# Kernel optimization log

Measured on AMD Instinct MI355X. Metric: run time of the kernel, lower is better.

## Reference

```python
import jax, jax.numpy as jnp
import numpy as np

B, S, D = 2, 2048, 2048
NH, NG = 16, 4          # q heads, groups
KVH = NH // NG          # kv heads = 4
HD = D // NH            # head dim = 128
ROPE_THETA = 10000.0


def _rope(t, cos, sin):
    """Rotate pairs along last dim. t: [B,S,D]; cos/sin: [S, D//2]."""
    tr = t.reshape(t.shape[:-1] + (-1, 2))  # [B,S,D/2,2] complex pairs (llama layout)
    xr, xi = tr[..., 0], tr[..., 1]
    c = cos[None, :, :]
    s = sin[None, :, :]
    yr = xr * c - xi * s
    yi = xr * s + xi * c
    return jnp.stack([yr, yi], axis=-1).reshape(t.shape)


def setup_inputs() -> dict:
    key = jax.random.key(0)
    k0, k1, k2, k3, k4 = jax.random.split(key, 5)
    scale = 1.0 / np.sqrt(D)
    x = jax.random.normal(k0, (B, S, D), jnp.float32)
    Wq = jax.random.normal(k1, (D, D), jnp.float32) * scale          # torch Linear: (out,in)
    Wk = jax.random.normal(k2, (D // NG, D), jnp.float32) * scale
    Wv = jax.random.normal(k3, (D // NG, D), jnp.float32) * scale
    Wo = jax.random.normal(k4, (D, D), jnp.float32) * scale
    mask = jnp.triu(jnp.ones((S, S), bool), k=1)[None, None]          # causal: True = masked
    return {"x": x, "Wq": Wq, "Wk": Wk, "Wv": Wv, "Wo": Wo, "mask": mask}


def reference(x, Wq, Wk, Wv, Wo, mask):
    b, s, d = x.shape
    q = x @ Wq.T                                  # [B,S,D]
    k = x @ Wk.T                                  # [B,S,D/NG]
    v = x @ Wv.T
    # repeat_kv: [B,S,KVH,HD] -> repeat each kv head NG times -> [B,S,NH,HD]
    k = jnp.repeat(k.reshape(b, s, KVH, HD), NG, axis=2).reshape(b, s, d)
    v = jnp.repeat(v.reshape(b, s, KVH, HD), NG, axis=2).reshape(b, s, d)
    # RoPE with freqs precomputed over the FULL hidden dim (as in source)
    freqs = 1.0 / (ROPE_THETA ** (jnp.arange(0, d, 2, dtype=jnp.float32) / d))  # [D/2]
    ang = jnp.arange(s, dtype=jnp.float32)[:, None] * freqs[None, :]            # [S,D/2]
    cos, sin = jnp.cos(ang), jnp.sin(ang)
    q = _rope(q, cos, sin)
    k = _rope(k, cos, sin)
    # split heads: [B,NH,S,HD]
    qh = q.reshape(b, s, NH, HD).transpose(0, 2, 1, 3)
    kh = k.reshape(b, s, NH, HD).transpose(0, 2, 1, 3)
    vh = v.reshape(b, s, NH, HD).transpose(0, 2, 1, 3)
    # NOTE: source scales by sqrt(hidden_dim), not sqrt(head_dim)
    scores = jnp.einsum('bhqd,bhkd->bhqk', qh, kh) / jnp.sqrt(jnp.float32(d))
    scores = jnp.where(mask, -jnp.inf, scores)
    probs = jax.nn.softmax(scores, axis=-1)
    out = jnp.einsum('bhqk,bhkd->bhqd', probs, vh)
    out = out.transpose(0, 2, 1, 3).reshape(b, s, d)
    return out @ Wo.T  # dropout is identity in eval
```

## Files before the change

kernel.cpp:

```cpp
#include <hip/hip_runtime.h>
#include <hip/hip_bf16.h>
#include <stdint.h>

typedef unsigned short u16;
typedef u16 u16x4 __attribute__((ext_vector_type(4)));
typedef unsigned u32x4 __attribute__((ext_vector_type(4)));
typedef __bf16 bf16x8 __attribute__((ext_vector_type(8)));
typedef float f32x4 __attribute__((ext_vector_type(4)));
typedef float f32x16 __attribute__((ext_vector_type(16)));

#define DEVI __device__ __forceinline__

DEVI u16 f2b(float f) {
  __hip_bfloat16 h = __float2bfloat16(f);
  return __builtin_bit_cast(u16, h);
}

DEVI unsigned pk2(float lo, float hi) {
  return (unsigned)f2b(lo) | ((unsigned)f2b(hi) << 16);
}

DEVI f32x4 mfma16(bf16x8 a, bf16x8 b, f32x4 c) {
  return __builtin_amdgcn_mfma_f32_16x16x32_bf16(a, b, c, 0, 0, 0);
}

DEVI f32x16 mfma32(bf16x8 a, bf16x8 b, f32x16 c) {
  return __builtin_amdgcn_mfma_f32_32x32x16_bf16(a, b, c, 0, 0, 0);
}

DEVI void gld_lds16(const u16* g, u16* l) {
  __builtin_amdgcn_global_load_lds(
      (const __attribute__((address_space(1))) unsigned int*)g,
      (__attribute__((address_space(3))) unsigned int*)l, 16, 0, 0);
}

__global__ void cvt_all(const float4* __restrict__ x, const float4* __restrict__ wq,
                        const float4* __restrict__ wk, const float4* __restrict__ wv,
                        const float4* __restrict__ wo,
                        u16x4* __restrict__ xb, u16x4* __restrict__ wqb,
                        u16x4* __restrict__ wkb, u16x4* __restrict__ wvb,
                        u16x4* __restrict__ wob) {
  long i = (long)blockIdx.x * 256 + threadIdx.x;
  const float4* src; u16x4* dst; long o;
  if (i < 2097152)      { src = x;  dst = xb;  o = i; }
  else if (i < 3145728) { src = wq; dst = wqb; o = i - 2097152; }
  else if (i < 3407872) { src = wk; dst = wkb; o = i - 3145728; }
  else if (i < 3670016) { src = wv; dst = wvb; o = i - 3407872; }
  else                  { src = wo; dst = wob; o = i - 3670016; }
  float4 v = src[o];
  u16x4 r = { f2b(v.x), f2b(v.y), f2b(v.z), f2b(v.w) };
  dst[o] = r;
}

__global__ void rope_table(float2* __restrict__ csT) {
  int i = blockIdx.x * 256 + threadIdx.x;
  int s = i >> 10, p = i & 1023;
  float freq = exp2f((float)p * -0.012976281620653759f);
  float ang = (float)s * freq;
  float sv, cv;
  __sincosf(ang, &sv, &cv);
  csT[i] = make_float2(cv, sv);
}

__global__ __launch_bounds__(256)
void gemm_qkv(const u16* __restrict__ A, const u16* __restrict__ wq,
              const u16* __restrict__ wk, const u16* __restrict__ wv,
              const float2* __restrict__ csT, u16* __restrict__ Qh,
              u16* __restrict__ Kh, u16* __restrict__ Vtp) {
  __shared__ __align__(16) u16 lds[3][8192];
  const int tid = threadIdx.x;
  const int lane = tid & 63;
  const int w = tid >> 6;
  const int wr = w >> 1, wc = w & 1;
  const int x = blockIdx.x, m0 = blockIdx.y << 7, n0 = x << 7;
  const int K = 2048;

  const u16* Bw;
  int mode;
  if (x < 16)      { Bw = wq + (size_t)n0 * K;          mode = 0; }
  else if (x < 20) { Bw = wk + (size_t)(n0 - 2048) * K; mode = 1; }
  else             { Bw = wv + (size_t)(n0 - 2560) * K; mode = 2; }

  const int srow = tid >> 2;
  const int cs = (tid & 3) ^ ((srow >> 1) & 3);
  const int p4 = srow >> 4, pl = srow & 15;
  const int prow = (pl << 1) | (p4 & 1) | ((p4 & 2) << 4);
  const int bsrc = (mode == 2) ? srow : prow;
  const u16* ga0 = A + (size_t)(m0 + srow) * K + (cs << 3);
  const u16* gb0 = Bw + (size_t)bsrc * K + (cs << 3);
  const size_t rstep = (size_t)64 * K;

  f32x4 acc[4][4] = {};
  const int nk = K >> 5;

#define QKV_STAGE(buf, ks)                                        \
  {                                                               \
    u16* l0 = &lds[buf][tid << 3];                                \
    const u16* ga_ = ga0 + ((size_t)(ks) << 5);                   \
    const u16* gb_ = gb0 + ((size_t)(ks) << 5);                   \
    gld_lds16(ga_, l0);                                           \
    gld_lds16(ga_ + rstep, l0 + 2048);                            \
    gld_lds16(gb_, l0 + 4096);                                    \
    gld_lds16(gb_ + rstep, l0 + 6144);                            \
  }

  QKV_STAGE(0, 0);
  QKV_STAGE(1, 1);

  const int l15 = lane & 15;
  const int lg = lane >> 4;
  const int ch8 = (lg ^ ((l15 >> 1) & 3)) << 3;
  const int abase = (((wr << 6) + l15) << 5) + ch8;
  const int bbase = 4096 + (((wc << 6) + l15) << 5) + ch8;

  int bufc = 0;
  for (int kt = 0; kt < nk; ++kt) {
    asm volatile("s_waitcnt vmcnt(4)" ::: "memory");
    __builtin_amdgcn_sched_barrier(0);
    __builtin_amdgcn_s_barrier();
    {
      const int ts = (kt + 2 < nk) ? kt + 2 : nk - 1;
      const int bufn = bufc ? bufc - 1 : 2;
      QKV_STAGE(bufn, ts);
    }
    const u16* lb_ = lds[bufc];
    bf16x8 af[4], bfr[4];
#pragma unroll
    for (int mi = 0; mi < 4; ++mi)
      af[mi] = *(const bf16x8*)&lb_[abase + (mi << 9)];
#pragma unroll
    for (int ni = 0; ni < 4; ++ni)
      bfr[ni] = *(const bf16x8*)&lb_[bbase + (ni << 9)];
    __builtin_amdgcn_s_setprio(1);
#pragma unroll
    for (int mi = 0; mi < 4; ++mi)
#pragma unroll
      for (int ni = 0; ni < 4; ++ni)
        acc[mi][ni] = mfma16(af[mi], bfr[ni], acc[mi][ni]);
    __builtin_amdgcn_s_setprio(0);
    bufc = (bufc == 2) ? 0 : bufc + 1;
  }
  asm volatile("s_waitcnt vmcnt(0)" ::: "memory");
#undef QKV_STAGE

  const int crow = (lane >> 4) << 2;
  if (mode == 0) {
    const float SCL = 0.022097086912079608f * 1.4426950408889634f;
    const int h = x;
    const int qb = (wc << 6) + (l15 << 1);
    const int tb = (n0 >> 1) + (wc << 5) + l15;
#pragma unroll
    for (int mi = 0; mi < 4; ++mi)
#pragma unroll
      for (int rr = 0; rr < 4; ++rr) {
        int row = m0 + (wr << 6) + (mi << 4) + crow + rr;
        int s = row & 2047, b = row >> 11;
        float2 cA = csT[(s << 10) + tb];
        float2 cB = csT[(s << 10) + tb + 16];
        float v0 = acc[mi][0][rr], v1 = acc[mi][1][rr];
        float v2 = acc[mi][2][rr], v3 = acc[mi][3][rr];
        unsigned lo = pk2((v0 * cA.x - v1 * cA.y) * SCL, (v0 * cA.y + v1 * cA.x) * SCL);
        unsigned hi = pk2((v2 * cB.x - v3 * cB.y) * SCL, (v2 * cB.y + v3 * cB.x) * SCL);
        u16* dst = &Qh[((size_t)(b * 16 + h) * 2048 + s) * 128 + qb];
        *(unsigned*)dst = lo;
        *(unsigned*)(dst + 32) = hi;
      }
  } else if (mode == 1) {
    const int kvh = x - 16;
    const int qb = (wc << 6) + (l15 << 1);
#pragma unroll
    for (int mi = 0; mi < 4; ++mi)
#pragma unroll
      for (int rr = 0; rr < 4; ++rr) {
        int row = m0 + (wr << 6) + (mi << 4) + crow + rr;
        int s = row & 2047, b = row >> 11;
        float v0 = acc[mi][0][rr], v1 = acc[mi][1][rr];
        float v2 = acc[mi][2][rr], v3 = acc[mi][3][rr];
#pragma unroll
        for (int g = 0; g < 4; ++g) {
          int h = (kvh << 2) + g;
          int tb = (h << 6) + (wc << 5) + l15;
          float2 cA = csT[(s << 10) + tb];
          float2 cB = csT[(s << 10) + tb + 16];
          unsigned lo = pk2(v0 * cA.x - v1 * cA.y, v0 * cA.y + v1 * cA.x);
          unsigned hi = pk2(v2 * cB.x - v3 * cB.y, v2 * cB.y + v3 * cB.x);
          u16* dst = &Kh[((size_t)(b * 16 + h) * 2048 + s) * 128 + qb];
          *(unsigned*)dst = lo;
          *(unsigned*)(dst + 32) = hi;
        }
      }
  } else {
    const int ccol = l15;
#pragma unroll
    for (int mi = 0; mi < 4; ++mi) {
      int sg = m0 + (wr << 6) + (mi << 4) + crow;
      int b = sg >> 11, s = sg & 2047;
#pragma unroll
      for (int ni = 0; ni < 4; ++ni) {
        int n = (n0 - 2560) + (wc << 6) + (ni << 4) + ccol;
        u16x4 pk = { f2b(acc[mi][ni][0]), f2b(acc[mi][ni][1]),
                     f2b(acc[mi][ni][2]), f2b(acc[mi][ni][3]) };
        *(u16x4*)&Vtp[((size_t)((b << 2) + (n >> 7)) * 128 + (n & 127)) * 2048 + s] = pk;
      }
    }
  }
}

__global__ __launch_bounds__(256)
void gemm_bt(const u16* __restrict__ A, const u16* __restrict__ Bw,
             float* __restrict__ C, int M, int N, int K) {
  __shared__ __align__(16) u16 lds[3][8192];
  const int tid = threadIdx.x;
  const int lane = tid & 63;
  const int w = tid >> 6;
  const int wr = w >> 1, wc = w & 1;
  const int m0 = blockIdx.y << 7, n0 = blockIdx.x << 7;

  const int srow = tid >> 2;
  const int cs = (tid & 3) ^ ((srow >> 1) & 3);
  const u16* ga0 = A + (size_t)(m0 + srow) * K + (cs << 3);
  const u16* gb0 = Bw + (size_t)(n0 + srow) * K + (cs << 3);
  const size_t rstep = (size_t)64 * K;

  f32x4 acc[4][4] = {};
  const int nk = K >> 5;

#define BT_STAGE(buf, ks)                                         \
  {                                                               \
    u16* l0 = &lds[buf][tid << 3];                                \
    const u16* ga_ = ga0 + ((size_t)(ks) << 5);                   \
    const u16* gb_ = gb0 + ((size_t)(ks) << 5);                   \
    gld_lds16(ga_, l0);                                           \
    gld_lds16(ga_ + rstep, l0 + 2048);                            \
    gld_lds16(gb_, l0 + 4096);                                    \
    gld_lds16(gb_ + rstep, l0 + 6144);                            \
  }

  BT_STAGE(0, 0);
  BT_STAGE(1, 1);

  const int l15 = lane & 15;
  const int lg = lane >> 4;
  const int ch8 = (lg ^ ((l15 >> 1) & 3)) << 3;
  const int abase = (((wr << 6) + l15) << 5) + ch8;
  const int bbase = 4096 + (((wc << 6) + l15) << 5) + ch8;

  int bufc = 0;
  for (int kt = 0; kt < nk; ++kt) {
    asm volatile("s_waitcnt vmcnt(4)" ::: "memory");
    __builtin_amdgcn_sched_barrier(0);
    __builtin_amdgcn_s_barrier();
    {
      const int ts = (kt + 2 < nk) ? kt + 2 : nk - 1;
      const int bufn = bufc ? bufc - 1 : 2;
      BT_STAGE(bufn, ts);
    }
    const u16* lb_ = lds[bufc];
    bf16x8 af[4], bfr[4];
#pragma unroll
    for (int mi = 0; mi < 4; ++mi)
      af[mi] = *(const bf16x8*)&lb_[abase + (mi << 9)];
#pragma unroll
    for (int ni = 0; ni < 4; ++ni)
      bfr[ni] = *(const bf16x8*)&lb_[bbase + (ni << 9)];
    __builtin_amdgcn_s_setprio(1);
#pragma unroll
    for (int mi = 0; mi < 4; ++mi)
#pragma unroll
      for (int ni = 0; ni < 4; ++ni)
        acc[mi][ni] = mfma16(af[mi], bfr[ni], acc[mi][ni]);
    __builtin_amdgcn_s_setprio(0);
    bufc = (bufc == 2) ? 0 : bufc + 1;
  }
  asm volatile("s_waitcnt vmcnt(0)" ::: "memory");
#undef BT_STAGE

  const int crow = (lane >> 4) << 2;
  const int ccol = lane & 15;
#pragma unroll
  for (int mi = 0; mi < 4; ++mi) {
    int row = m0 + (wr << 6) + (mi << 4) + crow;
#pragma unroll
    for (int ni = 0; ni < 4; ++ni) {
      int col = n0 + (wc << 6) + (ni << 4) + ccol;
#pragma unroll
      for (int rr = 0; rr < 4; ++rr)
        C[(size_t)(row + rr) * N + col] = acc[mi][ni][rr];
    }
  }
}

__global__ __launch_bounds__(256, 2)
void attn_kernel(const u16* __restrict__ Qh, const u16* __restrict__ Kh,
                 const u16* __restrict__ Vt, u16* __restrict__ attnO) {
  __shared__ __align__(16) u16 lds[3][8192];
  const int tid = threadIdx.x, lane = tid & 63, w = tid >> 6;
  const int bid = blockIdx.x;
  const int x = bid & 7, j = bid >> 3;
  const int half = j >> 5, jj = j & 31;
  const int bh = (x << 2) + (jj >> 4) + (half << 1);
  const int r = jj & 15;
  const int qt = half ? r : 15 - r;
  const int h = bh & 15, b = bh >> 4;

  const int qi = lane & 31, hi = lane >> 5;
  const int q0 = (qt << 7) + (w << 5);
  const int qabs = q0 + qi;

  const u16* Qp = Qh + (size_t)(b * 16 + h) * 262144;
  const u16* Kp = Kh + (size_t)(b * 16 + h) * 262144;
  const u16* Vp = Vt + (size_t)((b << 2) + (h >> 2)) * 262144;

  bf16x8 qf[8];
#pragma unroll
  for (int kc = 0; kc < 8; ++kc)
    qf[kc] = *(const bf16x8*)&Qp[(size_t)qabs * 128 + kc * 16 + hi * 8];

  const int kRow = tid >> 4;
  const int kCl = ((tid & 15) ^ (kRow & 7)) << 3;
  const int vRow = tid >> 2;
  const int vCl = ((tid & 3) ^ ((tid >> 3) & 3)) << 3;
  const int ldsoff = tid << 3;

  f32x16 ot[4] = {};
  float mrow = -1e30f, lsum = 0.f;
  const int nt = (qt << 2) + 4;
  const int nt_w = (qt << 2) + w + 1;
  const int swq = qi & 7, swv = (qi >> 1) & 3;

#pragma unroll
  for (int pt = 0; pt < 2; ++pt) {
    u16* bb = (u16*)lds[pt];
    gld_lds16(Kp + (size_t)((pt << 5) + kRow) * 128 + kCl, bb + ldsoff);
    gld_lds16(Kp + (size_t)((pt << 5) + kRow + 16) * 128 + kCl, bb + ldsoff + 2048);
    gld_lds16(Vp + (size_t)vRow * 2048 + (pt << 5) + vCl, bb + 4096 + ldsoff);
    gld_lds16(Vp + (size_t)(vRow + 64) * 2048 + (pt << 5) + vCl, bb + 4096 + ldsoff + 2048);
  }

  int bufc = 0;
  for (int t = 0; t < nt; ++t) {
    asm volatile("s_waitcnt vmcnt(4)" ::: "memory");
    __builtin_amdgcn_sched_barrier(0);
    __builtin_amdgcn_s_barrier();
    {
      const int ts = (t + 2 < nt) ? t + 2 : nt - 1;
      const int bufn = bufc ? bufc - 1 : 2;
      u16* bb = (u16*)lds[bufn];
      gld_lds16(Kp + (size_t)((ts << 5) + kRow) * 128 + kCl, bb + ldsoff);
      gld_lds16(Kp + (size_t)((ts << 5) + kRow + 16) * 128 + kCl, bb + ldsoff + 2048);
      gld_lds16(Vp + (size_t)vRow * 2048 + (ts << 5) + vCl, bb + 4096 + ldsoff);
      gld_lds16(Vp + (size_t)(vRow + 64) * 2048 + (ts << 5) + vCl, bb + 4096 + ldsoff + 2048);
    }
    if (t < nt_w) {
      const u16* kb_ = &lds[bufc][0];
      const u16* vb_ = &lds[bufc][4096];
      f32x16 st = {};
      __builtin_amdgcn_s_setprio(1);
#pragma unroll
      for (int kc = 0; kc < 8; ++kc) {
        bf16x8 kf = *(const bf16x8*)&kb_[(qi << 7) + ((((kc << 1) + hi) ^ swq) << 3)];
        st = mfma32(kf, qf[kc], st);
      }
      __builtin_amdgcn_s_setprio(0);

      if (t == nt_w - 1) {
        const int kb0 = t << 5;
#pragma unroll
        for (int reg = 0; reg < 16; ++reg) {
          int kk = kb0 + (reg & 3) + ((reg >> 2) << 3) + (hi << 2);
          if (kk > qabs) st[reg] = -1e30f;
        }
      }

      float tmax = st[0];
#pragma unroll
      for (int reg = 1; reg < 16; ++reg) tmax = fmaxf(tmax, st[reg]);
      tmax = fmaxf(tmax, __shfl_xor(tmax, 32));

      if (__any(tmax - mrow > 11.5f)) {
        float nm = fmaxf(mrow, tmax);
        float al = __builtin_amdgcn_exp2f(mrow - nm);
        mrow = nm;
        lsum *= al;
#pragma unroll
        for (int db = 0; db < 4; ++db)
#pragma unroll
          for (int reg = 0; reg < 16; ++reg) ot[db][reg] *= al;
      }

      float psum = 0.f;
#pragma unroll
      for (int reg = 0; reg < 16; ++reg) {
        st[reg] = __builtin_amdgcn_exp2f(st[reg] - mrow);
        psum += st[reg];
      }
      psum += __shfl_xor(psum, 32);
      lsum += psum;

      bf16x8 pfrag[2];
#pragma unroll
      for (int bbp = 0; bbp < 2; ++bbp) {
        unsigned x0 = pk2(st[8 * bbp + 0], st[8 * bbp + 1]);
        unsigned x1 = pk2(st[8 * bbp + 2], st[8 * bbp + 3]);
        unsigned y0 = pk2(st[8 * bbp + 4], st[8 * bbp + 5]);
        unsigned y1 = pk2(st[8 * bbp + 6], st[8 * bbp + 7]);
        asm("v_permlane32_swap_b32 %0, %1" : "+v"(x0), "+v"(y0));
        asm("v_permlane32_swap_b32 %0, %1" : "+v"(x1), "+v"(y1));
        u32x4 uw = { x0, x1, y0, y1 };
        pfrag[bbp] = __builtin_bit_cast(bf16x8, uw);
      }

      __builtin_amdgcn_s_setprio(1);
#pragma unroll
      for (int db = 0; db < 4; ++db) {
        const u16* vr = &vb_[((db << 5) + qi) << 5];
#pragma unroll
        for (int ks = 0; ks < 2; ++ks) {
          bf16x8 vf = *(const bf16x8*)&vr[((((ks << 1) + hi)) ^ swv) << 3];
          ot[db] = mfma32(vf, pfrag[ks], ot[db]);
        }
      }
      __builtin_amdgcn_s_setprio(0);
    }
    bufc = (bufc == 2) ? 0 : bufc + 1;
  }

  float inv = 1.f / lsum;
  u16* rowp = attnO + (size_t)(b * 2048 + qabs) * 2048 + h * 128 + (hi << 2);
#pragma unroll
  for (int db = 0; db < 4; ++db)
#pragma unroll
    for (int mg = 0; mg < 4; ++mg) {
      u16x4 pkv = { f2b(ot[db][4 * mg + 0] * inv), f2b(ot[db][4 * mg + 1] * inv),
                    f2b(ot[db][4 * mg + 2] * inv), f2b(ot[db][4 * mg + 3] * inv) };
      *(u16x4*)&rowp[(db << 5) + (mg << 3)] = pkv;
    }
}

extern "C" void kernel_launch(void* const* d_in, const int* in_sizes, int n_in,
                              void* d_out, int out_size, void* d_ws, size_t ws_size,
                              hipStream_t stream) {
  const float* x  = (const float*)d_in[0];
  const float* Wq = (const float*)d_in[1];
  const float* Wk = (const float*)d_in[2];
  const float* Wv = (const float*)d_in[3];
  const float* Wo = (const float*)d_in[4];
  float* out = (float*)d_out;
  char* ws = (char*)d_ws;

  u16*    xb   = (u16*)(ws + 0);
  u16*    wqb  = (u16*)(ws + 16777216);
  u16*    wkb  = (u16*)(ws + 25165824);
  u16*    wvb  = (u16*)(ws + 27262976);
  u16*    wob  = (u16*)(ws + 29360128);
  float2* csT  = (float2*)(ws + 37748736);
  u16*    Qhp  = (u16*)(ws + 54525952);
  u16*    Khp  = (u16*)(ws + 71303168);
  u16*    Vtp  = (u16*)(ws + 88080384);
  u16*    attnb= (u16*)(ws + 92274688);

  cvt_all<<<18432, 256, 0, stream>>>((const float4*)x, (const float4*)Wq,
                                     (const float4*)Wk, (const float4*)Wv,
                                     (const float4*)Wo, (u16x4*)xb, (u16x4*)wqb,
                                     (u16x4*)wkb, (u16x4*)wvb, (u16x4*)wob);
  rope_table<<<8192, 256, 0, stream>>>(csT);
  gemm_qkv<<<dim3(24, 32), 256, 0, stream>>>(xb, wqb, wkb, wvb, csT, Qhp, Khp, Vtp);
  attn_kernel<<<512, 256, 0, stream>>>(Qhp, Khp, Vtp, attnb);
  gemm_bt<<<dim3(16, 32), 256, 0, stream>>>(attnb, wob, out, 4096, 2048, 2048);
}
```

Before: 217.8 us.

## Enlarge GEMM tiles to 256x256 with 512 threads and merge prep kernels

Both the QKV projection and output projection GEMMs move from 128x128 tiles with 4 waves to 256x256 tiles with 8 waves. Each wave now holds an 8x4 accumulator grid, which doubles operand reuse per LDS load, and LDS per block grows to 96 KB. The cost is a much smaller grid (192 and 128 blocks on a 256-CU part), so many CUs sit idle. The rope table and bf16 conversion kernels are also merged into one launch to save a launch gap.

Measured after the change: 216.8 us. Within noise of the previous version (-0.4%).

```diff
diff --git a/kernel.cpp b/kernel.cpp
--- a/kernel.cpp
+++ b/kernel.cpp
@@ -34,13 +34,24 @@
       (__attribute__((address_space(3))) unsigned int*)l, 16, 0, 0);
 }
 
-__global__ void cvt_all(const float4* __restrict__ x, const float4* __restrict__ wq,
-                        const float4* __restrict__ wk, const float4* __restrict__ wv,
-                        const float4* __restrict__ wo,
-                        u16x4* __restrict__ xb, u16x4* __restrict__ wqb,
-                        u16x4* __restrict__ wkb, u16x4* __restrict__ wvb,
-                        u16x4* __restrict__ wob) {
-  long i = (long)blockIdx.x * 256 + threadIdx.x;
+__global__ void prep(const float4* __restrict__ x, const float4* __restrict__ wq,
+                     const float4* __restrict__ wk, const float4* __restrict__ wv,
+                     const float4* __restrict__ wo,
+                     u16x4* __restrict__ xb, u16x4* __restrict__ wqb,
+                     u16x4* __restrict__ wkb, u16x4* __restrict__ wvb,
+                     u16x4* __restrict__ wob, float2* __restrict__ csT) {
+  long bid = blockIdx.x;
+  if (bid < 8192) {
+    int i = (int)bid * 256 + threadIdx.x;
+    int s = i >> 10, p = i & 1023;
+    float freq = exp2f((float)p * -0.012976281620653759f);
+    float ang = (float)s * freq;
+    float sv, cv;
+    __sincosf(ang, &sv, &cv);
+    csT[i] = make_float2(cv, sv);
+    return;
+  }
+  long i = (bid - 8192) * 256 + threadIdx.x;
   const float4* src; u16x4* dst; long o;
   if (i < 2097152)      { src = x;  dst = xb;  o = i; }
   else if (i < 3145728) { src = wq; dst = wqb; o = i - 2097152; }
@@ -52,45 +63,35 @@
   dst[o] = r;
 }
 
-__global__ void rope_table(float2* __restrict__ csT) {
-  int i = blockIdx.x * 256 + threadIdx.x;
-  int s = i >> 10, p = i & 1023;
-  float freq = exp2f((float)p * -0.012976281620653759f);
-  float ang = (float)s * freq;
-  float sv, cv;
-  __sincosf(ang, &sv, &cv);
-  csT[i] = make_float2(cv, sv);
-}
-
-__global__ __launch_bounds__(256)
+__global__ __launch_bounds__(512)
 void gemm_qkv(const u16* __restrict__ A, const u16* __restrict__ wq,
               const u16* __restrict__ wk, const u16* __restrict__ wv,
               const float2* __restrict__ csT, u16* __restrict__ Qh,
               u16* __restrict__ Kh, u16* __restrict__ Vtp) {
-  __shared__ __align__(16) u16 lds[3][8192];
+  __shared__ __align__(16) u16 lds[3][16384];
   const int tid = threadIdx.x;
   const int lane = tid & 63;
   const int w = tid >> 6;
-  const int wr = w >> 1, wc = w & 1;
-  const int x = blockIdx.x, m0 = blockIdx.y << 7, n0 = x << 7;
+  const int wr = w >> 2, wc = w & 3;
+  const int x = blockIdx.x, m0 = blockIdx.y << 8, n0 = x << 8;
   const int K = 2048;
 
   const u16* Bw;
   int mode;
-  if (x < 16)      { Bw = wq + (size_t)n0 * K;          mode = 0; }
-  else if (x < 20) { Bw = wk + (size_t)(n0 - 2048) * K; mode = 1; }
+  if (x < 8)       { Bw = wq + (size_t)n0 * K;          mode = 0; }
+  else if (x < 10) { Bw = wk + (size_t)(n0 - 2048) * K; mode = 1; }
   else             { Bw = wv + (size_t)(n0 - 2560) * K; mode = 2; }
 
   const int srow = tid >> 2;
   const int cs = (tid & 3) ^ ((srow >> 1) & 3);
-  const int p4 = srow >> 4, pl = srow & 15;
-  const int prow = (pl << 1) | (p4 & 1) | ((p4 & 2) << 4);
+  const int p = srow & 63, p4 = p >> 4, pl = p & 15;
+  const int prow = (srow & ~63) | (pl << 1) | (p4 & 1) | ((p4 & 2) << 4);
   const int bsrc = (mode == 2) ? srow : prow;
   const u16* ga0 = A + (size_t)(m0 + srow) * K + (cs << 3);
   const u16* gb0 = Bw + (size_t)bsrc * K + (cs << 3);
-  const size_t rstep = (size_t)64 * K;
-
-  f32x4 acc[4][4] = {};
+  const size_t rstep = (size_t)128 * K;
+
+  f32x4 acc[8][4] = {};
   const int nk = K >> 5;
 
 #define QKV_STAGE(buf, ks)                                        \
@@ -99,9 +100,9 @@
     const u16* ga_ = ga0 + ((size_t)(ks) << 5);                   \
     const u16* gb_ = gb0 + ((size_t)(ks) << 5);                   \
     gld_lds16(ga_, l0);                                           \
-    gld_lds16(ga_ + rstep, l0 + 2048);                            \
-    gld_lds16(gb_, l0 + 4096);                                    \
-    gld_lds16(gb_ + rstep, l0 + 6144);                            \
+    gld_lds16(ga_ + rstep, l0 + 4096);                            \
+    gld_lds16(gb_, l0 + 8192);                                    \
+    gld_lds16(gb_ + rstep, l0 + 12288);                           \
   }
 
   QKV_STAGE(0, 0);
@@ -110,8 +111,8 @@
   const int l15 = lane & 15;
   const int lg = lane >> 4;
   const int ch8 = (lg ^ ((l15 >> 1) & 3)) << 3;
-  const int abase = (((wr << 6) + l15) << 5) + ch8;
-  const int bbase = 4096 + (((wc << 6) + l15) << 5) + ch8;
+  const int arow0 = (wr << 7) + l15;
+  const int brow0 = (wc << 6) + l15;
 
   int bufc = 0;
   for (int kt = 0; kt < nk; ++kt) {
@@ -123,17 +124,18 @@
       const int bufn = bufc ? bufc - 1 : 2;
       QKV_STAGE(bufn, ts);
     }
-    const u16* lb_ = lds[bufc];
-    bf16x8 af[4], bfr[4];
-#pragma unroll
-    for (int mi = 0; mi < 4; ++mi)
-      af[mi] = *(const bf16x8*)&lb_[abase + (mi << 9)];
+    const u16* la = &lds[bufc][0];
+    const u16* lb = &lds[bufc][8192];
+    bf16x8 af[8], bfr[4];
+#pragma unroll
+    for (int mi = 0; mi < 8; ++mi)
+      af[mi] = *(const bf16x8*)&la[((arow0 + (mi << 4)) << 5) + ch8];
 #pragma unroll
     for (int ni = 0; ni < 4; ++ni)
-      bfr[ni] = *(const bf16x8*)&lb_[bbase + (ni << 9)];
+      bfr[ni] = *(const bf16x8*)&lb[((brow0 + (ni << 4)) << 5) + ch8];
     __builtin_amdgcn_s_setprio(1);
 #pragma unroll
-    for (int mi = 0; mi < 4; ++mi)
+    for (int mi = 0; mi < 8; ++mi)
 #pragma unroll
       for (int ni = 0; ni < 4; ++ni)
         acc[mi][ni] = mfma16(af[mi], bfr[ni], acc[mi][ni]);
@@ -146,14 +148,14 @@
   const int crow = (lane >> 4) << 2;
   if (mode == 0) {
     const float SCL = 0.022097086912079608f * 1.4426950408889634f;
-    const int h = x;
-    const int qb = (wc << 6) + (l15 << 1);
-    const int tb = (n0 >> 1) + (wc << 5) + l15;
-#pragma unroll
-    for (int mi = 0; mi < 4; ++mi)
+    const int h = (x << 1) + (wc >> 1);
+    const int hd0 = ((wc & 1) << 6) + (l15 << 1);
+    const int tb = (h << 6) + ((wc & 1) << 5) + l15;
+#pragma unroll
+    for (int mi = 0; mi < 8; ++mi)
 #pragma unroll
       for (int rr = 0; rr < 4; ++rr) {
-        int row = m0 + (wr << 6) + (mi << 4) + crow + rr;
+        int row = m0 + (wr << 7) + (mi << 4) + crow + rr;
         int s = row & 2047, b = row >> 11;
         float2 cA = csT[(s << 10) + tb];
         float2 cB = csT[(s << 10) + tb + 16];
@@ -161,43 +163,42 @@
         float v2 = acc[mi][2][rr], v3 = acc[mi][3][rr];
         unsigned lo = pk2((v0 * cA.x - v1 * cA.y) * SCL, (v0 * cA.y + v1 * cA.x) * SCL);
         unsigned hi = pk2((v2 * cB.x - v3 * cB.y) * SCL, (v2 * cB.y + v3 * cB.x) * SCL);
-        u16* dst = &Qh[((size_t)(b * 16 + h) * 2048 + s) * 128 + qb];
+        u16* dst = &Qh[((size_t)(b * 16 + h) * 2048 + s) * 128 + hd0];
         *(unsigned*)dst = lo;
         *(unsigned*)(dst + 32) = hi;
       }
   } else if (mode == 1) {
-    const int kvh = x - 16;
-    const int qb = (wc << 6) + (l15 << 1);
-#pragma unroll
-    for (int mi = 0; mi < 4; ++mi)
+    const int kvh = ((x - 8) << 1) + (wc >> 1);
+    const int hd0 = ((wc & 1) << 6) + (l15 << 1);
+#pragma unroll
+    for (int mi = 0; mi < 8; ++mi)
 #pragma unroll
       for (int rr = 0; rr < 4; ++rr) {
-        int row = m0 + (wr << 6) + (mi << 4) + crow + rr;
+        int row = m0 + (wr << 7) + (mi << 4) + crow + rr;
         int s = row & 2047, b = row >> 11;
         float v0 = acc[mi][0][rr], v1 = acc[mi][1][rr];
         float v2 = acc[mi][2][rr], v3 = acc[mi][3][rr];
 #pragma unroll
         for (int g = 0; g < 4; ++g) {
           int h = (kvh << 2) + g;
-          int tb = (h << 6) + (wc << 5) + l15;
+          int tb = (h << 6) + ((wc & 1) << 5) + l15;
           float2 cA = csT[(s << 10) + tb];
           float2 cB = csT[(s << 10) + tb + 16];
           unsigned lo = pk2(v0 * cA.x - v1 * cA.y, v0 * cA.y + v1 * cA.x);
           unsigned hi = pk2(v2 * cB.x - v3 * cB.y, v2 * cB.y + v3 * cB.x);
-          u16* dst = &Kh[((size_t)(b * 16 + h) * 2048 + s) * 128 + qb];
+          u16* dst = &Kh[((size_t)(b * 16 + h) * 2048 + s) * 128 + hd0];
           *(unsigned*)dst = lo;
           *(unsigned*)(dst + 32) = hi;
         }
       }
   } else {
-    const int ccol = l15;
-#pragma unroll
-    for (int mi = 0; mi < 4; ++mi) {
-      int sg = m0 + (wr << 6) + (mi << 4) + crow;
+#pragma unroll
+    for (int mi = 0; mi < 8; ++mi) {
+      int sg = m0 + (wr << 7) + (mi << 4) + crow;
       int b = sg >> 11, s = sg & 2047;
 #pragma unroll
       for (int ni = 0; ni < 4; ++ni) {
-        int n = (n0 - 2560) + (wc << 6) + (ni << 4) + ccol;
+        int n = ((x - 10) << 8) + (wc << 6) + (ni << 4) + l15;
         u16x4 pk = { f2b(acc[mi][ni][0]), f2b(acc[mi][ni][1]),
                      f2b(acc[mi][ni][2]), f2b(acc[mi][ni][3]) };
         *(u16x4*)&Vtp[((size_t)((b << 2) + (n >> 7)) * 128 + (n & 127)) * 2048 + s] = pk;
@@ -206,23 +207,23 @@
   }
 }
 
-__global__ __launch_bounds__(256)
+__global__ __launch_bounds__(512)
 void gemm_bt(const u16* __restrict__ A, const u16* __restrict__ Bw,
              float* __restrict__ C, int M, int N, int K) {
-  __shared__ __align__(16) u16 lds[3][8192];
+  __shared__ __align__(16) u16 lds[3][16384];
   const int tid = threadIdx.x;
   const int lane = tid & 63;
   const int w = tid >> 6;
-  const int wr = w >> 1, wc = w & 1;
-  const int m0 = blockIdx.y << 7, n0 = blockIdx.x << 7;
+  const int wr = w >> 2, wc = w & 3;
+  const int m0 = blockIdx.y << 8, n0 = blockIdx.x << 8;
 
   const int srow = tid >> 2;
   const int cs = (tid & 3) ^ ((srow >> 1) & 3);
   const u16* ga0 = A + (size_t)(m0 + srow) * K + (cs << 3);
   const u16* gb0 = Bw + (size_t)(n0 + srow) * K + (cs << 3);
-  const size_t rstep = (size_t)64 * K;
-
-  f32x4 acc[4][4] = {};
+  const size_t rstep = (size_t)128 * K;
+
+  f32x4 acc[8][4] = {};
   const int nk = K >> 5;
 
 #define BT_STAGE(buf, ks)                                         \
@@ -231,9 +232,9 @@
     const u16* ga_ = ga0 + ((size_t)(ks) << 5);                   \
     const u16* gb_ = gb0 + ((size_t)(ks) << 5);                   \
     gld_lds16(ga_, l0);                                           \
-    gld_lds16(ga_ + rstep, l0 + 2048);                            \
-    gld_lds16(gb_, l0 + 4096);                                    \
-    gld_lds16(gb_ + rstep, l0 + 6144);                            \
+    gld_lds16(ga_ + rstep, l0 + 4096);                            \
+    gld_lds16(gb_, l0 + 8192);                                    \
+    gld_lds16(gb_ + rstep, l0 + 12288);                           \
   }
 
   BT_STAGE(0, 0);
@@ -242,8 +243,8 @@
   const int l15 = lane & 15;
   const int lg = lane >> 4;
   const int ch8 = (lg ^ ((l15 >> 1) & 3)) << 3;
-  const int abase = (((wr << 6) + l15) << 5) + ch8;
-  const int bbase = 4096 + (((wc << 6) + l15) << 5) + ch8;
+  const int arow0 = (wr << 7) + l15;
+  const int brow0 = (wc << 6) + l15;
 
   int bufc = 0;
   for (int kt = 0; kt < nk; ++kt) {
@@ -255,17 +256,18 @@
       const int bufn = bufc ? bufc - 1 : 2;
       BT_STAGE(bufn, ts);
     }
-    const u16* lb_ = lds[bufc];
-    bf16x8 af[4], bfr[4];
-#pragma unroll
-    for (int mi = 0; mi < 4; ++mi)
-      af[mi] = *(const bf16x8*)&lb_[abase + (mi << 9)];
+    const u16* la = &lds[bufc][0];
+    const u16* lb = &lds[bufc][8192];
+    bf16x8 af[8], bfr[4];
+#pragma unroll
+    for (int mi = 0; mi < 8; ++mi)
+      af[mi] = *(const bf16x8*)&la[((arow0 + (mi << 4)) << 5) + ch8];
 #pragma unroll
     for (int ni = 0; ni < 4; ++ni)
-      bfr[ni] = *(const bf16x8*)&lb_[bbase + (ni << 9)];
+      bfr[ni] = *(const bf16x8*)&lb[((brow0 + (ni << 4)) << 5) + ch8];
     __builtin_amdgcn_s_setprio(1);
 #pragma unroll
-    for (int mi = 0; mi < 4; ++mi)
+    for (int mi = 0; mi < 8; ++mi)
 #pragma unroll
       for (int ni = 0; ni < 4; ++ni)
         acc[mi][ni] = mfma16(af[mi], bfr[ni], acc[mi][ni]);
@@ -276,13 +278,12 @@
 #undef BT_STAGE
 
   const int crow = (lane >> 4) << 2;
-  const int ccol = lane & 15;
-#pragma unroll
-  for (int mi = 0; mi < 4; ++mi) {
-    int row = m0 + (wr << 6) + (mi << 4) + crow;
+#pragma unroll
+  for (int mi = 0; mi < 8; ++mi) {
+    int row = m0 + (wr << 7) + (mi << 4) + crow;
 #pragma unroll
     for (int ni = 0; ni < 4; ++ni) {
-      int col = n0 + (wc << 6) + (ni << 4) + ccol;
+      int col = n0 + (wc << 6) + (ni << 4) + l15;
 #pragma unroll
       for (int rr = 0; rr < 4; ++rr)
         C[(size_t)(row + rr) * N + col] = acc[mi][ni][rr];
@@ -459,12 +460,11 @@
   u16*    Vtp  = (u16*)(ws + 88080384);
   u16*    attnb= (u16*)(ws + 92274688);
 
-  cvt_all<<<18432, 256, 0, stream>>>((const float4*)x, (const float4*)Wq,
-                                     (const float4*)Wk, (const float4*)Wv,
-                                     (const float4*)Wo, (u16x4*)xb, (u16x4*)wqb,
-                                     (u16x4*)wkb, (u16x4*)wvb, (u16x4*)wob);
-  rope_table<<<8192, 256, 0, stream>>>(csT);
-  gemm_qkv<<<dim3(24, 32), 256, 0, stream>>>(xb, wqb, wkb, wvb, csT, Qhp, Khp, Vtp);
+  prep<<<26624, 256, 0, stream>>>((const float4*)x, (const float4*)Wq,
+                                  (const float4*)Wk, (const float4*)Wv,
+                                  (const float4*)Wo, (u16x4*)xb, (u16x4*)wqb,
+                                  (u16x4*)wkb, (u16x4*)wvb, (u16x4*)wob, csT);
+  gemm_qkv<<<dim3(12, 16), 512, 0, stream>>>(xb, wqb, wkb, wvb, csT, Qhp, Khp, Vtp);
   attn_kernel<<<512, 256, 0, stream>>>(Qhp, Khp, Vtp, attnb);
-  gemm_bt<<<dim3(16, 32), 256, 0, stream>>>(attnb, wob, out, 4096, 2048, 2048);
-}
+  gemm_bt<<<dim3(8, 16), 512, 0, stream>>>(attnb, wob, out, 4096, 2048, 2048);
+}
```
